# Kernel tuning notes

Hardware: AMD Instinct MI355X
Metric: run time of the kernel (lower is better)

The kernel has to match this reference:

```python
import jax, jax.numpy as jnp
import numpy as np

N = 50000       # population nodes
E = 1_600_000   # edges per edge type
F_IN = 2000     # flattened individual-graph embedding (100*20)
D = 20          # hidden channels per TransformerConv head (heads=1)
NEG_SLOPE = 0.01
BN_EPS = 1e-5


def setup_inputs() -> dict:
    key = jax.random.key(0)
    ks = jax.random.split(key, 24)
    features = jax.random.normal(ks[0], (N, F_IN), jnp.float32)
    same_index = jax.random.randint(ks[1], (2, E), 0, N, dtype=jnp.int64)
    diff_index = jax.random.randint(ks[2], (2, E), 0, N, dtype=jnp.int64)
    s0 = 1.0 / np.sqrt(F_IN)
    s1 = 1.0 / np.sqrt(D)
    # layer 0 conv params, stacked over the 2 edge types (same, diff)
    W0q = jax.random.normal(ks[3], (2, F_IN, D), jnp.float32) * s0
    W0k = jax.random.normal(ks[4], (2, F_IN, D), jnp.float32) * s0
    W0v = jax.random.normal(ks[5], (2, F_IN, D), jnp.float32) * s0
    W0s = jax.random.normal(ks[6], (2, F_IN, D), jnp.float32) * s0
    b0q = jnp.zeros((2, D)); b0k = jnp.zeros((2, D))
    b0v = jnp.zeros((2, D)); b0s = jnp.zeros((2, D))
    # layers 1..3 conv params: [layer, edge_type, D, D]
    Wq = jax.random.normal(ks[7], (3, 2, D, D), jnp.float32) * s1
    Wk = jax.random.normal(ks[8], (3, 2, D, D), jnp.float32) * s1
    Wv = jax.random.normal(ks[9], (3, 2, D, D), jnp.float32) * s1
    Ws = jax.random.normal(ks[10], (3, 2, D, D), jnp.float32) * s1
    bq = jnp.zeros((3, 2, D)); bk = jnp.zeros((3, 2, D))
    bv = jnp.zeros((3, 2, D)); bs = jnp.zeros((3, 2, D))
    w1 = jnp.full((4,), 0.8, jnp.float32)
    w2 = jnp.full((4,), 0.2, jnp.float32)
    bn_gamma = jnp.ones((4, D), jnp.float32)
    bn_beta = jnp.zeros((4, D), jnp.float32)
    Wout = jax.random.normal(ks[11], (4 * D, 2), jnp.float32) / np.sqrt(4 * D)
    bout = jnp.zeros((2,), jnp.float32)
    return dict(features=features, same_index=same_index, diff_index=diff_index,
                W0q=W0q, b0q=b0q, W0k=W0k, b0k=b0k, W0v=W0v, b0v=b0v, W0s=W0s, b0s=b0s,
                Wq=Wq, bq=bq, Wk=Wk, bk=bk, Wv=Wv, bv=bv, Ws=Ws, bs=bs,
                w1=w1, w2=w2, bn_gamma=bn_gamma, bn_beta=bn_beta, Wout=Wout, bout=bout)


def _tconv(x, edge_index, Wq, bq, Wk, bk, Wv, bv, Ws, bs):
    """PyG TransformerConv, heads=1, concat=True, root_weight=True, no edge_attr."""
    src, dst = edge_index[0], edge_index[1]
    q = x @ Wq + bq   # [N, D]
    k = x @ Wk + bk
    v = x @ Wv + bv
    logits = jnp.einsum('ed,ed->e', q[dst], k[src]) / jnp.sqrt(jnp.float32(D))  # [E]
    m = jax.ops.segment_max(logits, dst, num_segments=N)
    m = jnp.where(jnp.isfinite(m), m, jnp.float32(0.0))  # nodes with no in-edges
    e = jnp.exp(logits - m[dst])
    z = jax.ops.segment_sum(e, dst, num_segments=N)
    alpha = e / (z[dst] + 1e-16)  # PyG softmax epsilon
    agg = jax.ops.segment_sum(alpha[:, None] * v[src], dst, num_segments=N)  # [N, D]
    return agg + x @ Ws + bs  # skip (root) connection


def _bn(x, gamma, beta):
    mu = x.mean(axis=0)
    var = x.var(axis=0)
    return (x - mu) * jax.lax.rsqrt(var + BN_EPS) * gamma + beta


def reference(features, same_index, diff_index,
              W0q, b0q, W0k, b0k, W0v, b0v, W0s, b0s,
              Wq, bq, Wk, bk, Wv, bv, Ws, bs,
              w1, w2, bn_gamma, bn_beta, Wout, bout):
    x = features
    fcs = []
    for l in range(4):
        if l == 0:
            p_same = (W0q[0], b0q[0], W0k[0], b0k[0], W0v[0], b0v[0], W0s[0], b0s[0])
            p_diff = (W0q[1], b0q[1], W0k[1], b0k[1], W0v[1], b0v[1], W0s[1], b0s[1])
        else:
            i = l - 1
            p_same = (Wq[i, 0], bq[i, 0], Wk[i, 0], bk[i, 0], Wv[i, 0], bv[i, 0], Ws[i, 0], bs[i, 0])
            p_diff = (Wq[i, 1], bq[i, 1], Wk[i, 1], bk[i, 1], Wv[i, 1], bv[i, 1], Ws[i, 1], bs[i, 1])
        x1 = _tconv(x, same_index, *p_same)
        x2 = _tconv(x, diff_index, *p_diff)
        t = w1[l] + w2[l]
        x = (w1[l] / t) * x1 + (w2[l] / t) * x2
        x = _bn(x, bn_gamma[l], bn_beta[l])
        x = jax.nn.leaky_relu(x, NEG_SLOPE)
        fcs.append(x)
    fc = jnp.concatenate(fcs, axis=-1)  # [N, 80]
    return fc @ Wout + bout  # [N, 2]
```

## Files before the change

kernel.cpp:

```cpp
#include <hip/hip_runtime.h>
#include <math.h>

#define N_NODES 50000
#define E_EDGES 1600000
#define F_IN    2000
#define D       20
#define NCOL    160
#define KPAD    2016
#define NBNP    64

#define INV_SQRT_D 0.22360679774997896f

typedef __bf16 bf16x8 __attribute__((ext_vector_type(8)));
typedef __bf16 bf16x4 __attribute__((ext_vector_type(4)));
typedef float  f32x4  __attribute__((ext_vector_type(4)));


__global__ void pack_kernel(
    const float* __restrict__ W0q, const float* __restrict__ W0k,
    const float* __restrict__ W0v, const float* __restrict__ W0s,
    const float* __restrict__ b0q, const float* __restrict__ b0k,
    const float* __restrict__ b0v, const float* __restrict__ b0s,
    const float* __restrict__ Wq,  const float* __restrict__ Wk,
    const float* __restrict__ Wv,  const float* __restrict__ Ws_,
    const float* __restrict__ bq,  const float* __restrict__ bk,
    const float* __restrict__ bv,  const float* __restrict__ bs_,
    __bf16* __restrict__ B0, float* __restrict__ bias0,
    float* __restrict__ WL, float* __restrict__ biasL,
    float* __restrict__ bnp, int* __restrict__ deg)
{
  long idx = (long)blockIdx.x * blockDim.x + threadIdx.x;
  if (idx < (long)NCOL*KPAD) {
    int col = (int)(idx / KPAD), k = (int)(idx % KPAD);
    int et = col / 80, r = col % 80, mat = r / 20, d = r % 20;
    const float* w = (mat==0)?W0q:(mat==1)?W0s:(mat==2)?W0k:W0v;
    float v = (k < F_IN) ? w[((size_t)et*F_IN + k)*D + d] : 0.f;
    B0[idx] = (__bf16)v;
    return;
  }
  idx -= (long)NCOL*KPAD;
  if (idx < 160) {
    int col = (int)idx;
    int et = col / 80, r = col % 80, mat = r / 20, d = r % 20;
    const float* b = (mat==0)?b0q:(mat==1)?b0s:(mat==2)?b0k:b0v;
    bias0[col] = b[et*D + d];
    return;
  }
  idx -= 160;
  if (idx < 9600) {
    int l = (int)(idx / 3200), rem = (int)(idx % 3200);
    int k = rem / NCOL, col = rem % NCOL;
    int et = col / 80, r = col % 80, mat = r / 20, d = r % 20;
    const float* w = (mat==0)?Wq:(mat==1)?Ws_:(mat==2)?Wk:Wv;
    WL[idx] = w[(((size_t)l*2 + et)*D + k)*D + d];
    return;
  }
  idx -= 9600;
  if (idx < 480) {
    int l = (int)(idx / NCOL), col = (int)(idx % NCOL);
    int et = col / 80, r = col % 80, mat = r / 20, d = r % 20;
    const float* b = (mat==0)?bq:(mat==1)?bs_:(mat==2)?bk:bv;
    biasL[idx] = b[(l*2 + et)*D + d];
    return;
  }
  idx -= 480;
  if (idx < 4*NBNP*40) { bnp[idx] = 0.f; return; }
  idx -= 4*NBNP*40;
  if (idx < 2*N_NODES) { deg[idx] = 0; return; }
}

#define SC_EPT 16
#define SC_CHUNK (256*SC_EPT)

__global__ void hist_kernel(const int* __restrict__ same, const int* __restrict__ diff,
                            int* __restrict__ deg)
{
  const int part  = blockIdx.x & 7;
  const int chunk = blockIdx.x >> 3;
  const int lo = part * (N_NODES/8);
  const int hi = lo + (N_NODES/8);
  const long i0 = (long)chunk * SC_CHUNK + threadIdx.x;
#pragma unroll
  for (int it = 0; it < SC_EPT; ++it) {
    long i = i0 + (long)it*256;
    if (i >= 2L*E_EDGES) break;
    int et = (i >= E_EDGES) ? 1 : 0;
    long e = i - (long)et*E_EDGES;
    const int* ix = et ? diff : same;
    int dst = ix[E_EDGES + e];
    if (dst >= lo && dst < hi)
      atomicAdd(&deg[(size_t)et*N_NODES + dst], 1);
  }
}

__global__ void scan_kernel(const int* __restrict__ deg,
                            int* __restrict__ rowptr0, int* __restrict__ rowptr1,
                            int* __restrict__ next0, int* __restrict__ next1)
{
  const int et = blockIdx.x;
  const int* dg = deg + (size_t)et*N_NODES;
  int* rp = et ? rowptr1 : rowptr0;
  int* np = et ? next1 : next0;
  __shared__ int part[1024];
  const int t = threadIdx.x;
  const int per = (N_NODES + 1023) / 1024;
  const int b = t * per;
  const int e = (b + per < N_NODES) ? (b + per) : N_NODES;
  int s = 0;
  for (int i = b; i < e; i++) s += dg[i];
  part[t] = s;
  __syncthreads();
  for (int o = 1; o < 1024; o <<= 1) {
    int v = (t >= o) ? part[t-o] : 0;
    __syncthreads();
    part[t] += v;
    __syncthreads();
  }
  int run = (t == 0) ? 0 : part[t-1];
  for (int i = b; i < e; i++) {
    rp[i] = run; np[i] = run;
    run += dg[i];
  }
  if (t == 0) rp[N_NODES] = part[1023];
}

__global__ void scatter_kernel(const int* __restrict__ same, const int* __restrict__ diff,
                               int* __restrict__ next0, int* __restrict__ next1,
                               int* __restrict__ adj0, int* __restrict__ adj1)
{
  const int part  = blockIdx.x & 7;
  const int chunk = blockIdx.x >> 3;
  const int lo = part * (N_NODES/8);
  const int hi = lo + (N_NODES/8);
  const long i0 = (long)chunk * SC_CHUNK + threadIdx.x;
#pragma unroll
  for (int it = 0; it < SC_EPT; ++it) {
    long i = i0 + (long)it*256;
    if (i >= 2L*E_EDGES) break;
    int et = (i >= E_EDGES) ? 1 : 0;
    long e = i - (long)et*E_EDGES;
    const int* ix = et ? diff : same;
    int dst = ix[E_EDGES + e];
    if (dst >= lo && dst < hi) {
      int src = ix[e];
      int* np  = et ? next1 : next0;
      int* adj = et ? adj1  : adj0;
      int pos = atomicAdd(&np[dst], 1);
      adj[pos] = src;
    }
  }
}

__launch_bounds__(256)
__global__ void gemm0_mfma(const float* __restrict__ A,
                           const __bf16* __restrict__ Bt,
                           const float* __restrict__ bias,
                           __bf16* __restrict__ QS,
                           __bf16* __restrict__ KV0, __bf16* __restrict__ KV1)
{
  __shared__ __bf16 as[64*32];
  const int t    = threadIdx.x;
  const int lane = t & 63;
  const int wid  = t >> 6;
  const int wr   = wid >> 1;
  const int wc   = wid & 1;
  const int rb0  = blockIdx.x * 64;

  const int srow = t >> 2;
  const int skc  = (t & 3) * 8;
  const int arow = rb0 + srow;
  const float* aptr = A + (size_t)arow * F_IN;

  const int lrow = lane & 15;
  const int lkb  = (lane >> 4) * 8;

  f32x4 acc[2][5];
#pragma unroll
  for (int i = 0; i < 2; i++)
#pragma unroll
    for (int j = 0; j < 5; j++) acc[i][j] = (f32x4){0.f,0.f,0.f,0.f};

  float4 p0, p1;
  auto loadA = [&](int k0) {
    int k = k0 + skc;
    if (arow < N_NODES) {
      if (k + 8 <= F_IN) {
        p0 = *(const float4*)(aptr + k);
        p1 = *(const float4*)(aptr + k + 4);
      } else {
        float tmp[8];
#pragma unroll
        for (int i = 0; i < 8; i++) tmp[i] = (k + i < F_IN) ? aptr[k + i] : 0.f;
        p0 = make_float4(tmp[0],tmp[1],tmp[2],tmp[3]);
        p1 = make_float4(tmp[4],tmp[5],tmp[6],tmp[7]);
      }
    } else {
      p0 = make_float4(0,0,0,0); p1 = p0;
    }
  };

  loadA(0);
  for (int s = 0; s < 63; s++) {
    bf16x8 h;
    h[0]=(__bf16)p0.x; h[1]=(__bf16)p0.y; h[2]=(__bf16)p0.z; h[3]=(__bf16)p0.w;
    h[4]=(__bf16)p1.x; h[5]=(__bf16)p1.y; h[6]=(__bf16)p1.z; h[7]=(__bf16)p1.w;
    *(bf16x8*)&as[srow*32 + skc] = h;
    __syncthreads();
    if (s + 1 < 63) loadA((s + 1) * 32);

    bf16x8 af[2];
#pragma unroll
    for (int rf = 0; rf < 2; rf++)
      af[rf] = *(bf16x8*)&as[(wr*32 + rf*16 + lrow)*32 + lkb];
    bf16x8 bfr[5];
#pragma unroll
    for (int cf = 0; cf < 5; cf++)
      bfr[cf] = *(const bf16x8*)(Bt + (size_t)(wc*80 + cf*16 + lrow)*KPAD + s*32 + lkb);
#pragma unroll
    for (int rf = 0; rf < 2; rf++)
#pragma unroll
      for (int cf = 0; cf < 5; cf++)
        acc[rf][cf] = __builtin_amdgcn_mfma_f32_16x16x32_bf16(af[rf], bfr[cf], acc[rf][cf], 0, 0, 0);
    __syncthreads();
  }

#pragma unroll
  for (int rf = 0; rf < 2; rf++) {
#pragma unroll
    for (int cf = 0; cf < 5; cf++) {
      int col = wc*80 + cf*16 + lrow;
      int et = col / 80, r = col % 80, mat = r / 20, d = r % 20;
      float bv = bias[col];
      __bf16* kvp = et ? KV1 : KV0;
#pragma unroll
      for (int j = 0; j < 4; j++) {
        int row = rb0 + wr*32 + rf*16 + (lane >> 4)*4 + j;
        if (row < N_NODES) {
          __bf16 val = (__bf16)(acc[rf][cf][j] + bv);
          if (mat < 2) QS[(size_t)row*80 + et*40 + mat*20 + d] = val;
          else         kvp[(size_t)row*64 + (mat-2)*20 + d]   = val;
        }
      }
    }
  }
}

__launch_bounds__(256)
__global__ void proj_small_kernel(const float* __restrict__ xp, const float* __restrict__ bnl,
                                  const float* __restrict__ gam, const float* __restrict__ bet,
                                  const float* __restrict__ W, const float* __restrict__ bias,
                                  __bf16* __restrict__ QS,
                                  __bf16* __restrict__ KV0, __bf16* __restrict__ KV1)
{
  __shared__ float ws[20*160];
  __shared__ float xs[16*20];
  __shared__ float Ac[20], Bc[20];
  const int t = threadIdx.x;
  const int n0 = blockIdx.x * 16;
#pragma unroll
  for (int i = 0; i < 13; i++) {
    int idx = t + i*256;
    if (idx < 3200) ws[idx] = W[idx];
  }
  if (t < 20) {
    float s1 = 0.f, s2 = 0.f;
    for (int s = 0; s < NBNP; s++) { s1 += bnl[s*40 + t]; s2 += bnl[s*40 + 20 + t]; }
    float mu  = s1 * (1.f/N_NODES);
    float var = s2 * (1.f/N_NODES) - mu*mu;
    float a = rsqrtf(var + 1e-5f) * gam[t];
    Ac[t] = a; Bc[t] = bet[t] - mu*a;
  }
  __syncthreads();
#pragma unroll
  for (int i = 0; i < 2; i++) {
    int idx = t + i*256;
    if (idx < 320) {
      int nl = idx / 20, k = idx % 20;
      int n = n0 + nl;
      float x = (n < N_NODES) ? xp[(size_t)n*D + k] : 0.f;
      float y = x*Ac[k] + Bc[k];
      xs[idx] = (y > 0.f) ? y : 0.01f*y;
    }
  }
  __syncthreads();
#pragma unroll
  for (int i = 0; i < 10; i++) {
    int idx = t + i*256;
    int nl = idx / NCOL, col = idx % NCOL;
    int n = n0 + nl;
    if (n < N_NODES) {
      float acc = bias[col];
#pragma unroll
      for (int k = 0; k < 20; k++) acc += xs[nl*20 + k] * ws[k*NCOL + col];
      int et = col / 80, r = col % 80, mat = r / 20, d = r % 20;
      __bf16 val = (__bf16)acc;
      if (mat < 2) QS[(size_t)n*80 + et*40 + mat*20 + d] = val;
      else         (et ? KV1 : KV0)[(size_t)n*64 + (mat-2)*20 + d] = val;
    }
  }
}

__launch_bounds__(256)
__global__ void attn_fused(const int* __restrict__ rp0, const int* __restrict__ adj0,
                           const int* __restrict__ rp1, const int* __restrict__ adj1,
                           const __bf16* __restrict__ QS,
                           const __bf16* __restrict__ KV0, const __bf16* __restrict__ KV1,
                           const float* __restrict__ w1, const float* __restrict__ w2, int l,
                           float* __restrict__ xpre, float* __restrict__ bnp)
{
  const int t    = threadIdx.x;
  const int wv   = t >> 6;
  const int lane = t & 63;
  const int half = lane >> 5;
  const int sl   = lane & 31;
  const int node = blockIdx.x*4 + wv;

  const int* rowptr = half ? rp1 : rp0;
  const int* adj    = half ? adj1 : adj0;
  const __bf16* kvb = half ? KV1 : KV0;
  const __bf16* rq  = QS + (size_t)node*80 + half*40;

  float qf[20];
  {
    bf16x8 q0 = *(const bf16x8*)(rq);
    bf16x8 q1 = *(const bf16x8*)(rq + 8);
    bf16x4 q2 = *(const bf16x4*)(rq + 16);
#pragma unroll
    for (int i = 0; i < 8; i++) { qf[i] = (float)q0[i]; qf[8+i] = (float)q1[i]; }
#pragma unroll
    for (int i = 0; i < 4; i++) qf[16+i] = (float)q2[i];
  }

  const int beg = rowptr[node], end = rowptr[node+1];
  float z = 0.f;
  float S[20];
#pragma unroll
  for (int d = 0; d < 20; d++) S[d] = 0.f;

  int i = beg + sl;
  for (; i + 32 < end; i += 64) {
    const int s0 = adj[i], s1 = adj[i+32];
    const __bf16* kva = kvb + (size_t)s0*64;
    const __bf16* kvc = kvb + (size_t)s1*64;
    bf16x8 a0 = *(const bf16x8*)(kva);
    bf16x8 a1 = *(const bf16x8*)(kva + 8);
    bf16x8 a2 = *(const bf16x8*)(kva + 16);
    bf16x8 a3 = *(const bf16x8*)(kva + 24);
    bf16x8 a4 = *(const bf16x8*)(kva + 32);
    bf16x8 b0 = *(const bf16x8*)(kvc);
    bf16x8 b1 = *(const bf16x8*)(kvc + 8);
    bf16x8 b2 = *(const bf16x8*)(kvc + 16);
    bf16x8 b3 = *(const bf16x8*)(kvc + 24);
    bf16x8 b4 = *(const bf16x8*)(kvc + 32);

    float d0 = 0.f, d1 = 0.f;
#pragma unroll
    for (int j = 0; j < 8; j++) { d0 += qf[j]*(float)a0[j];     d1 += qf[j]*(float)b0[j]; }
#pragma unroll
    for (int j = 0; j < 8; j++) { d0 += qf[8+j]*(float)a1[j];   d1 += qf[8+j]*(float)b1[j]; }
#pragma unroll
    for (int j = 0; j < 4; j++) { d0 += qf[16+j]*(float)a2[j];  d1 += qf[16+j]*(float)b2[j]; }
    const float w0 = __expf(fminf(d0*INV_SQRT_D, 80.f));
    const float w1v= __expf(fminf(d1*INV_SQRT_D, 80.f));
    z += w0 + w1v;
#pragma unroll
    for (int d = 0; d < 4; d++) S[d]     += w0*(float)a2[4+d] + w1v*(float)b2[4+d];
#pragma unroll
    for (int d = 0; d < 8; d++) S[4+d]   += w0*(float)a3[d]   + w1v*(float)b3[d];
#pragma unroll
    for (int d = 0; d < 8; d++) S[12+d]  += w0*(float)a4[d]   + w1v*(float)b4[d];
  }
  if (i < end) {
    const int s0 = adj[i];
    const __bf16* kva = kvb + (size_t)s0*64;
    bf16x8 a0 = *(const bf16x8*)(kva);
    bf16x8 a1 = *(const bf16x8*)(kva + 8);
    bf16x8 a2 = *(const bf16x8*)(kva + 16);
    bf16x8 a3 = *(const bf16x8*)(kva + 24);
    bf16x8 a4 = *(const bf16x8*)(kva + 32);
    float d0 = 0.f;
#pragma unroll
    for (int j = 0; j < 8; j++) d0 += qf[j]     * (float)a0[j];
#pragma unroll
    for (int j = 0; j < 8; j++) d0 += qf[8 + j] * (float)a1[j];
#pragma unroll
    for (int j = 0; j < 4; j++) d0 += qf[16 + j]* (float)a2[j];
    const float w0 = __expf(fminf(d0*INV_SQRT_D, 80.f));
    z += w0;
#pragma unroll
    for (int d = 0; d < 4; d++) S[d]     += w0*(float)a2[4+d];
#pragma unroll
    for (int d = 0; d < 8; d++) S[4+d]   += w0*(float)a3[d];
#pragma unroll
    for (int d = 0; d < 8; d++) S[12+d]  += w0*(float)a4[d];
  }

#pragma unroll
  for (int o = 16; o >= 1; o >>= 1) {
    z += __shfl_xor(z, o, 64);
#pragma unroll
    for (int d = 0; d < 20; d++) S[d] += __shfl_xor(S[d], o, 64);
  }

  const float inv = (z > 0.f) ? 1.f/z : 0.f;
  float outv[20];
  {
    bf16x4 s0 = *(const bf16x4*)(rq + 20);
    bf16x8 s1 = *(const bf16x8*)(rq + 24);
    bf16x8 s2 = *(const bf16x8*)(rq + 32);
#pragma unroll
    for (int i2 = 0; i2 < 4; i2++) outv[i2] = S[i2]*inv + (float)s0[i2];
#pragma unroll
    for (int i2 = 0; i2 < 8; i2++) { outv[4+i2]  = S[4+i2]*inv  + (float)s1[i2];
                                     outv[12+i2] = S[12+i2]*inv + (float)s2[i2]; }
  }

  const float wa = w1[l], wb = w2[l];
  const float c0 = wa/(wa+wb), c1 = wb/(wa+wb);
  const float cme = half ? c1 : c0;
  const float cot = half ? c0 : c1;
  float x[20];
#pragma unroll
  for (int d = 0; d < 20; d++) {
    float o2 = __shfl_xor(outv[d], 32, 64);
    x[d] = cme*outv[d] + cot*o2;
  }

  if (lane == 0) {
    float* xo = xpre + (size_t)node*D;
#pragma unroll
    for (int j = 0; j < 5; j++) {
      float4 o4 = make_float4(x[4*j], x[4*j+1], x[4*j+2], x[4*j+3]);
      *(float4*)(xo + 4*j) = o4;
    }
  }

  float v = x[0];
#pragma unroll
  for (int d = 1; d < 20; d++) v = (sl == d) ? x[d] : v;
  if (sl < 20) {
    float* slot = bnp + (size_t)((blockIdx.x*4 + wv) & (NBNP-1))*40;
    if (half == 0) atomicAdd(&slot[sl], v);
    else           atomicAdd(&slot[20 + sl], v*v);
  }
}

__launch_bounds__(256)
__global__ void final_kernel(const float* __restrict__ xpre4, const float* __restrict__ bnp,
                             const float* __restrict__ gam, const float* __restrict__ bet,
                             const float* __restrict__ Wout, const float* __restrict__ bout,
                             float* __restrict__ out)
{
  __shared__ float Ac[80], Bc[80], wlds[160];
  const int t = threadIdx.x;
  if (t < 80) {
    int l = t / 20, d = t % 20;
    const float* b = bnp + l*(NBNP*40);
    float s1 = 0.f, s2 = 0.f;
    for (int s = 0; s < NBNP; s++) { s1 += b[s*40 + d]; s2 += b[s*40 + 20 + d]; }
    float mu  = s1 * (1.f/N_NODES);
    float var = s2 * (1.f/N_NODES) - mu*mu;
    float a = rsqrtf(var + 1e-5f) * gam[t];
    Ac[t] = a; Bc[t] = bet[t] - mu*a;
  }
  if (t < 160) wlds[t] = Wout[t];
  __syncthreads();

  const int n = blockIdx.x*256 + t;
  if (n >= N_NODES) return;
  float a0 = bout[0], a1 = bout[1];
#pragma unroll
  for (int l = 0; l < 4; l++) {
    const float* base = xpre4 + (size_t)l*N_NODES*D + (size_t)n*D;
#pragma unroll
    for (int d = 0; d < D; d++) {
      int idx = l*20 + d;
      float y = base[d]*Ac[idx] + Bc[idx];
      y = (y > 0.f) ? y : 0.01f*y;
      a0 += y * wlds[idx*2 + 0];
      a1 += y * wlds[idx*2 + 1];
    }
  }
  out[n*2+0] = a0;
  out[n*2+1] = a1;
}

extern "C" void kernel_launch(void* const* d_in, const int* in_sizes, int n_in,
                              void* d_out, int out_size, void* d_ws, size_t ws_size,
                              hipStream_t stream)
{
  const float* feat = (const float*)d_in[0];
  const int*   same = (const int*)d_in[1];
  const int*   diff = (const int*)d_in[2];
  const float* W0q = (const float*)d_in[3];
  const float* b0q = (const float*)d_in[4];
  const float* W0k = (const float*)d_in[5];
  const float* b0k = (const float*)d_in[6];
  const float* W0v = (const float*)d_in[7];
  const float* b0v = (const float*)d_in[8];
  const float* W0s = (const float*)d_in[9];
  const float* b0s = (const float*)d_in[10];
  const float* Wq  = (const float*)d_in[11];
  const float* bq  = (const float*)d_in[12];
  const float* Wk  = (const float*)d_in[13];
  const float* bk  = (const float*)d_in[14];
  const float* Wv  = (const float*)d_in[15];
  const float* bv  = (const float*)d_in[16];
  const float* Ws_ = (const float*)d_in[17];
  const float* bs_ = (const float*)d_in[18];
  const float* w1  = (const float*)d_in[19];
  const float* w2  = (const float*)d_in[20];
  const float* gamma = (const float*)d_in[21];
  const float* beta  = (const float*)d_in[22];
  const float* Wout  = (const float*)d_in[23];
  const float* bout  = (const float*)d_in[24];

  float* wsf  = (float*)d_ws;
  __bf16*  QS    = (__bf16*)wsf;
  __bf16*  KV0   = (__bf16*)(wsf + 2000000);
  __bf16*  KV1   = (__bf16*)(wsf + 3600000);
  float*   XPRE4 = wsf + 5200000;
  __bf16*  B0bf  = (__bf16*)(wsf + 9200000);
  float*   BIAS0 = wsf + 9361280;
  float*   WL    = wsf + 9361440;
  float*   BIASL = wsf + 9371040;
  float*   BNP   = wsf + 9371520;
  int*     ib    = (int*)(wsf + 9381760);
  int* DEG  = ib;
  int* RP0  = ib + 100000;
  int* RP1  = ib + 150004;
  int* NX0  = ib + 200008;
  int* NX1  = ib + 250008;
  int* ADJ0 = ib + 300008;
  int* ADJ1 = ib + 1900008;

  const int packN = NCOL*KPAD + 160 + 9600 + 480 + 4*NBNP*40 + 2*N_NODES;
  pack_kernel<<<(packN + 255)/256, 256, 0, stream>>>(
      W0q, W0k, W0v, W0s, b0q, b0k, b0v, b0s,
      Wq, Wk, Wv, Ws_, bq, bk, bv, bs_,
      B0bf, BIAS0, WL, BIASL, BNP, DEG);

  const long nchunk = (2L*E_EDGES + SC_CHUNK - 1) / SC_CHUNK;
  hist_kernel<<<(int)(nchunk*8), 256, 0, stream>>>(same, diff, DEG);
  scan_kernel<<<2, 1024, 0, stream>>>(DEG, RP0, RP1, NX0, NX1);
  scatter_kernel<<<(int)(nchunk*8), 256, 0, stream>>>(same, diff, NX0, NX1, ADJ0, ADJ1);

  for (int l = 0; l < 4; l++) {
    if (l == 0)
      gemm0_mfma<<<(N_NODES + 63)/64, 256, 0, stream>>>(feat, B0bf, BIAS0, QS, KV0, KV1);
    else
      proj_small_kernel<<<(N_NODES + 15)/16, 256, 0, stream>>>(
          XPRE4 + (size_t)(l-1)*N_NODES*D, BNP + (l-1)*(NBNP*40),
          gamma + (l-1)*D, beta + (l-1)*D,
          WL + (size_t)(l-1)*3200, BIASL + (size_t)(l-1)*160, QS, KV0, KV1);

    attn_fused<<<N_NODES/4, 256, 0, stream>>>(
        RP0, ADJ0, RP1, ADJ1, QS, KV0, KV1, w1, w2, l,
        XPRE4 + (size_t)l*N_NODES*D, BNP + l*(NBNP*40));
  }

  final_kernel<<<(N_NODES + 255)/256, 256, 0, stream>>>(
      XPRE4, BNP, gamma, beta, Wout, bout, (float*)d_out);
}
```

Baseline: 977.1 us.

## Double-buffer gemm0 LDS tiles and use 16 lanes per edge type in attention

The layer-0 GEMM now keeps two LDS tiles and prefetches A two k-steps ahead, so only one barrier per iteration remains and global loads overlap the MFMA work. The attention kernel now gives each edge type of a node 16 lanes instead of 32, so each wavefront handles two nodes and half as many blocks are launched. With an average in-degree of about 32 per edge type, this is meant to cut idle lanes and the length of the shuffle reduction. In exchange it adds register pressure from the extra prefetch buffers and makes each lane walk more edges sequentially.

```diff
diff --git a/kernel.cpp b/kernel.cpp
--- a/kernel.cpp
+++ b/kernel.cpp
@@ -158,7 +158,7 @@
                            __bf16* __restrict__ QS,
                            __bf16* __restrict__ KV0, __bf16* __restrict__ KV1)
 {
-  __shared__ __bf16 as[64*32];
+  __shared__ __bf16 as[2][64*32];
   const int t    = threadIdx.x;
   const int lane = t & 63;
   const int wid  = t >> 6;
@@ -180,48 +180,60 @@
 #pragma unroll
     for (int j = 0; j < 5; j++) acc[i][j] = (f32x4){0.f,0.f,0.f,0.f};
 
-  float4 p0, p1;
-  auto loadA = [&](int k0) {
+  auto loadA = [&](int k0, float4& q0, float4& q1) {
     int k = k0 + skc;
     if (arow < N_NODES) {
       if (k + 8 <= F_IN) {
-        p0 = *(const float4*)(aptr + k);
-        p1 = *(const float4*)(aptr + k + 4);
+        q0 = *(const float4*)(aptr + k);
+        q1 = *(const float4*)(aptr + k + 4);
       } else {
         float tmp[8];
 #pragma unroll
         for (int i = 0; i < 8; i++) tmp[i] = (k + i < F_IN) ? aptr[k + i] : 0.f;
-        p0 = make_float4(tmp[0],tmp[1],tmp[2],tmp[3]);
-        p1 = make_float4(tmp[4],tmp[5],tmp[6],tmp[7]);
+        q0 = make_float4(tmp[0],tmp[1],tmp[2],tmp[3]);
+        q1 = make_float4(tmp[4],tmp[5],tmp[6],tmp[7]);
       }
     } else {
-      p0 = make_float4(0,0,0,0); p1 = p0;
+      q0 = make_float4(0,0,0,0); q1 = q0;
     }
   };
-
-  loadA(0);
+  auto cvtStore = [&](int buf, const float4& q0, const float4& q1) {
+    bf16x8 h;
+    h[0]=(__bf16)q0.x; h[1]=(__bf16)q0.y; h[2]=(__bf16)q0.z; h[3]=(__bf16)q0.w;
+    h[4]=(__bf16)q1.x; h[5]=(__bf16)q1.y; h[6]=(__bf16)q1.z; h[7]=(__bf16)q1.w;
+    *(bf16x8*)&as[buf][srow*32 + skc] = h;
+  };
+
+  float4 pa0, pa1, pb0, pb1;
+  loadA(0,  pa0, pa1);
+  loadA(32, pb0, pb1);
+  cvtStore(0, pa0, pa1);
+  __syncthreads();
+
   for (int s = 0; s < 63; s++) {
-    bf16x8 h;
-    h[0]=(__bf16)p0.x; h[1]=(__bf16)p0.y; h[2]=(__bf16)p0.z; h[3]=(__bf16)p0.w;
-    h[4]=(__bf16)p1.x; h[5]=(__bf16)p1.y; h[6]=(__bf16)p1.z; h[7]=(__bf16)p1.w;
-    *(bf16x8*)&as[srow*32 + skc] = h;
-    __syncthreads();
-    if (s + 1 < 63) loadA((s + 1) * 32);
-
+    const int cur = s & 1;
     bf16x8 af[2];
 #pragma unroll
     for (int rf = 0; rf < 2; rf++)
-      af[rf] = *(bf16x8*)&as[(wr*32 + rf*16 + lrow)*32 + lkb];
+      af[rf] = *(bf16x8*)&as[cur][(wr*32 + rf*16 + lrow)*32 + lkb];
     bf16x8 bfr[5];
 #pragma unroll
     for (int cf = 0; cf < 5; cf++)
       bfr[cf] = *(const bf16x8*)(Bt + (size_t)(wc*80 + cf*16 + lrow)*KPAD + s*32 + lkb);
+
+    if (s + 1 < 63) cvtStore(cur ^ 1, pb0, pb1);
+    if (s + 2 < 63) loadA((s + 2) * 32, pa0, pa1);
+
 #pragma unroll
     for (int rf = 0; rf < 2; rf++)
 #pragma unroll
       for (int cf = 0; cf < 5; cf++)
         acc[rf][cf] = __builtin_amdgcn_mfma_f32_16x16x32_bf16(af[rf], bfr[cf], acc[rf][cf], 0, 0, 0);
     __syncthreads();
+
+    float4 t0 = pa0, t1 = pa1;
+    pa0 = pb0; pa1 = pb1;
+    pb0 = t0;  pb1 = t1;
   }
 
 #pragma unroll
@@ -311,14 +323,15 @@
   const int t    = threadIdx.x;
   const int wv   = t >> 6;
   const int lane = t & 63;
-  const int half = lane >> 5;
-  const int sl   = lane & 31;
-  const int node = blockIdx.x*4 + wv;
-
-  const int* rowptr = half ? rp1 : rp0;
-  const int* adj    = half ? adj1 : adj0;
-  const __bf16* kvb = half ? KV1 : KV0;
-  const __bf16* rq  = QS + (size_t)node*80 + half*40;
+  const int g    = lane >> 4;
+  const int sl   = lane & 15;
+  const int et   = g & 1;
+  const int node = blockIdx.x*8 + wv*2 + (g >> 1);
+
+  const int* rowptr = et ? rp1 : rp0;
+  const int* adj    = et ? adj1 : adj0;
+  const __bf16* kvb = et ? KV1 : KV0;
+  const __bf16* rq  = QS + (size_t)node*80 + et*40;
 
   float qf[20];
   {
@@ -338,8 +351,8 @@
   for (int d = 0; d < 20; d++) S[d] = 0.f;
 
   int i = beg + sl;
-  for (; i + 32 < end; i += 64) {
-    const int s0 = adj[i], s1 = adj[i+32];
+  for (; i + 16 < end; i += 32) {
+    const int s0 = adj[i], s1 = adj[i+16];
     const __bf16* kva = kvb + (size_t)s0*64;
     const __bf16* kvc = kvb + (size_t)s1*64;
     bf16x8 a0 = *(const bf16x8*)(kva);
@@ -396,7 +409,7 @@
   }
 
 #pragma unroll
-  for (int o = 16; o >= 1; o >>= 1) {
+  for (int o = 8; o >= 1; o >>= 1) {
     z += __shfl_xor(z, o, 64);
 #pragma unroll
     for (int d = 0; d < 20; d++) S[d] += __shfl_xor(S[d], o, 64);
@@ -417,16 +430,16 @@
 
   const float wa = w1[l], wb = w2[l];
   const float c0 = wa/(wa+wb), c1 = wb/(wa+wb);
-  const float cme = half ? c1 : c0;
-  const float cot = half ? c0 : c1;
+  const float cme = et ? c1 : c0;
+  const float cot = et ? c0 : c1;
   float x[20];
 #pragma unroll
   for (int d = 0; d < 20; d++) {
-    float o2 = __shfl_xor(outv[d], 32, 64);
+    float o2 = __shfl_xor(outv[d], 16, 64);
     x[d] = cme*outv[d] + cot*o2;
   }
 
-  if (lane == 0) {
+  if (et == 0 && sl == 0) {
     float* xo = xpre + (size_t)node*D;
 #pragma unroll
     for (int j = 0; j < 5; j++) {
@@ -437,11 +450,18 @@
 
   float v = x[0];
 #pragma unroll
-  for (int d = 1; d < 20; d++) v = (sl == d) ? x[d] : v;
-  if (sl < 20) {
-    float* slot = bnp + (size_t)((blockIdx.x*4 + wv) & (NBNP-1))*40;
-    if (half == 0) atomicAdd(&slot[sl], v);
-    else           atomicAdd(&slot[20 + sl], v*v);
+  for (int d = 1; d < 16; d++) v = (sl == d) ? x[d] : v;
+  float v2 = x[16];
+#pragma unroll
+  for (int d = 1; d < 4; d++) v2 = (sl == d) ? x[16 + d] : v2;
+
+  float* slot = bnp + (size_t)(node & (NBNP-1))*40;
+  if (et == 0) {
+    atomicAdd(&slot[sl], v);
+    if (sl < 4) atomicAdd(&slot[16 + sl], v2);
+  } else {
+    atomicAdd(&slot[20 + sl], v*v);
+    if (sl < 4) atomicAdd(&slot[36 + sl], v2*v2);
   }
 }
 
@@ -554,7 +574,7 @@
           gamma + (l-1)*D, beta + (l-1)*D,
           WL + (size_t)(l-1)*3200, BIASL + (size_t)(l-1)*160, QS, KV0, KV1);
 
-    attn_fused<<<N_NODES/4, 256, 0, stream>>>(
+    attn_fused<<<N_NODES/8, 256, 0, stream>>>(
         RP0, ADJ0, RP1, ADJ1, QS, KV0, KV1, w1, w2, l,
         XPRE4 + (size_t)l*N_NODES*D, BNP + l*(NBNP*40));
   }
```

Result: no change. 977.3 us (+0.0%).
